# Kernel optimization log

Measured on AMD Instinct MI355X. Metric: run time of the kernel, lower is better.

## Reference

```python
import jax, jax.numpy as jnp
import numpy as np

B = 4096   # batch
C = 1024   # per-node channels


def setup_inputs() -> dict:
    key = jax.random.key(0)
    k0, k1, k2, k3, k4 = jax.random.split(key, 5)
    x0 = jax.random.normal(k0, (B, C), dtype=jnp.float32)
    x1 = jax.random.normal(k1, (B, C), dtype=jnp.float32)
    # per-edge DNet weights: edge_in=concat (2 heads -> 2C) -> matmul W -> edge_out=split (2 tails of C)
    scale = 0.02
    W0 = jax.random.normal(k2, (2 * C, 2 * C), dtype=jnp.float32) * scale
    W1 = jax.random.normal(k3, (2 * C, 2 * C), dtype=jnp.float32) * scale
    W2 = jax.random.normal(k4, (2 * C, 2 * C), dtype=jnp.float32) * scale
    return {"x0": x0, "x1": x1, "W0": W0, "W1": W1, "W2": W2}


def _edge(head_a, head_b, W):
    # MHD_concat over sorted head nodes (dim=1), DNet matmul, MHD_split into tail node channels
    z = jnp.concatenate([head_a, head_b], axis=1) @ W  # [B, 2C]
    return z[:, :C], z[:, C:]  # two tail tensors [B, C]


def reference(x0, x1, W0, W1, W2):
    # DAG routing in topological order (MHD_topological_sort of the role matrix):
    # edge0: heads (n0, n1) -> tails (n2, n3)
    # edge1: heads (n2, n3) -> tails (n4, n5)
    # edge2: heads (n4, n5) -> tails (n6, n7)
    # node_tail_func = 'sum' (single contribution per tail here)
    n2, n3 = _edge(x0, x1, W0)
    n4, n5 = _edge(n2, n3, W1)
    n6, n7 = _edge(n4, n5, W2)
    # output: concat of terminal nodes (sorted order)
    return jnp.concatenate([n6, n7], axis=1)  # [B, 2C]
```

## Files before the change

### kernel.cpp

```cpp
#include <hip/hip_runtime.h>
#include <hip/hip_bf16.h>
#include <stdint.h>

typedef __bf16 bf16;
typedef __bf16 bf16x8 __attribute__((ext_vector_type(8)));
typedef float f32x4 __attribute__((ext_vector_type(4)));

#define GAS __attribute__((address_space(1)))
#define LAS __attribute__((address_space(3)))

static constexpr int M = 4096;
static constexpr int N = 2048;
static constexpr int K = 2048;

static constexpr int BM = 128, BN = 256, BK = 64;
static constexpr int NT = K / BK;
static constexpr int A_ELE = BM * BK;
static constexpr int B_ELE = BN * BK;
static constexpr int BUF_ELE = A_ELE + B_ELE;

__device__ __forceinline__ void gload_lds16(const bf16* gsrc, bf16* ldst) {
    __builtin_amdgcn_global_load_lds((const GAS void*)gsrc, (LAS void*)ldst, 16, 0, 0);
}

__global__ __launch_bounds__(256) void prep_kernel(const float* __restrict__ x0,
                                                   const float* __restrict__ x1,
                                                   const float* __restrict__ W0,
                                                   const float* __restrict__ W1,
                                                   const float* __restrict__ W2,
                                                   bf16* __restrict__ A,
                                                   bf16* __restrict__ Wt0,
                                                   bf16* __restrict__ Wt1,
                                                   bf16* __restrict__ Wt2) {
    __shared__ bf16 tile[32][33];
    int bid = blockIdx.x;
    int tid = threadIdx.x;
    if (bid < 4096) {
        int idx = (bid * 256 + tid) * 8;
        int b = idx >> 11;
        int c = idx & 2047;
        const float* src = (c < 1024) ? (x0 + (size_t)b * 1024 + c)
                                      : (x1 + (size_t)b * 1024 + (c - 1024));
        float4 v0 = *reinterpret_cast<const float4*>(src);
        float4 v1 = *reinterpret_cast<const float4*>(src + 4);
        bf16x8 o;
        o[0] = (bf16)v0.x; o[1] = (bf16)v0.y; o[2] = (bf16)v0.z; o[3] = (bf16)v0.w;
        o[4] = (bf16)v1.x; o[5] = (bf16)v1.y; o[6] = (bf16)v1.z; o[7] = (bf16)v1.w;
        *reinterpret_cast<bf16x8*>(A + idx) = o;
    } else {
        int r = bid - 4096;
        int w = r >> 12;
        int t = r & 4095;
        const float* W  = (w == 0) ? W0  : (w == 1) ? W1  : W2;
        bf16*        Wt = (w == 0) ? Wt0 : (w == 1) ? Wt1 : Wt2;
        int n0 = (t & 63) * 32;
        int k0 = (t >> 6) * 32;
        int tx = tid & 31;
        int ty = tid >> 5;
        #pragma unroll
        for (int i = 0; i < 4; i++) {
            int k = ty + i * 8;
            tile[k][tx] = (bf16)W[(size_t)(k0 + k) * N + n0 + tx];
        }
        __syncthreads();
        #pragma unroll
        for (int i = 0; i < 4; i++) {
            int n = ty + i * 8;
            Wt[(size_t)(n0 + n) * K + k0 + tx] = tile[tx][n];
        }
    }
}

__device__ __forceinline__ void read_frags(const bf16* __restrict__ ba, const bf16* __restrict__ bb,
                                           int aoff, int boff, int slot,
                                           bf16x8 af[4], bf16x8 bv[4]) {
    #pragma unroll
    for (int mi = 0; mi < 4; mi++)
        af[mi] = *reinterpret_cast<const bf16x8*>(ba + aoff + mi * 1024 + slot);
    #pragma unroll
    for (int ni = 0; ni < 4; ni++)
        bv[ni] = *reinterpret_cast<const bf16x8*>(bb + boff + ni * 1024 + slot);
}

__device__ __forceinline__ void do_mfma16(const bf16x8 af[4], const bf16x8 bv[4], f32x4 acc[4][4]) {
    __builtin_amdgcn_s_setprio(1);
    #pragma unroll
    for (int mi = 0; mi < 4; mi++)
        #pragma unroll
        for (int ni = 0; ni < 4; ni++)
            acc[mi][ni] = __builtin_amdgcn_mfma_f32_16x16x32_bf16(af[mi], bv[ni], acc[mi][ni], 0, 0, 0);
    __builtin_amdgcn_s_setprio(0);
}

template <bool OUT_BF16>
__global__ __launch_bounds__(512, 2) void gemm1b_kernel(const bf16* __restrict__ A,
                                                        const bf16* __restrict__ Bt,
                                                        void* __restrict__ Cout) {
    __shared__ bf16 lds[3 * BUF_ELE];

    int bid = blockIdx.x;
    int cpx = gridDim.x >> 3;
    int swz = (bid & 7) * cpx + (bid >> 3);
    int tm = swz >> 3;
    int tn = swz & 7;

    int tid  = threadIdx.x;
    int wave = tid >> 6;
    int lane = tid & 63;
    int wr = wave >> 2;
    int wc = wave & 3;
    int fr = lane & 15;
    int fb = lane >> 4;

    int srow = wave * 8 + (lane >> 3);
    int scol = ((lane & 7) ^ (lane >> 3)) * 8;
    const bf16* aS = A  + (size_t)(tm * BM + srow) * K + scol;
    const bf16* bS = Bt + (size_t)(tn * BN + srow) * K + scol;
    int sdst = wave * 512;

    int aoff  = (wr * 64 + fr) * 64;
    int boff  = (wc * 64 + fr) * 64;
    int slot0 = ((fb) ^ (fr & 7)) * 8;
    int slot1 = ((4 | fb) ^ (fr & 7)) * 8;

    f32x4 acc[4][4] = {};

    auto STAGE = [&](int bi, int t) {
        bf16* ba = (bf16*)lds + bi * BUF_ELE;
        bf16* bb = ba + A_ELE;
        const bf16* a = aS + t * BK;
        const bf16* b = bS + t * BK;
        gload_lds16(a,           ba + sdst);
        gload_lds16(a + 64 * K,  ba + sdst + 4096);
        gload_lds16(b,           bb + sdst);
        gload_lds16(b + 64 * K,  bb + sdst + 4096);
        gload_lds16(b + 128 * K, bb + sdst + 8192);
        gload_lds16(b + 192 * K, bb + sdst + 12288);
    };

    STAGE(0, 0);
    STAGE(1, 1);
    asm volatile("s_waitcnt vmcnt(6)" ::: "memory");
    __builtin_amdgcn_s_barrier();

    bf16x8 af0[4], bv0[4], af1[4], bv1[4];
    int cur = 0;
    for (int t = 0; t < NT - 2; ++t) {
        const bf16* ba = (const bf16*)lds + cur * BUF_ELE;
        const bf16* bb = ba + A_ELE;
        int sb = cur + 2; if (sb >= 3) sb -= 3;

        read_frags(ba, bb, aoff, boff, slot0, af0, bv0);
        read_frags(ba, bb, aoff, boff, slot1, af1, bv1);
        STAGE(sb, t + 2);
        asm volatile("s_waitcnt lgkmcnt(8)" ::: "memory");
        do_mfma16(af0, bv0, acc);
        asm volatile("s_waitcnt lgkmcnt(0)" ::: "memory");
        do_mfma16(af1, bv1, acc);
        asm volatile("s_waitcnt vmcnt(6)" ::: "memory");
        __builtin_amdgcn_s_barrier();
        cur = cur + 1; if (cur >= 3) cur -= 3;
    }
    {
        const bf16* ba = (const bf16*)lds + cur * BUF_ELE;
        const bf16* bb = ba + A_ELE;
        read_frags(ba, bb, aoff, boff, slot0, af0, bv0);
        read_frags(ba, bb, aoff, boff, slot1, af1, bv1);
        asm volatile("s_waitcnt lgkmcnt(8)" ::: "memory");
        do_mfma16(af0, bv0, acc);
        asm volatile("s_waitcnt lgkmcnt(0)" ::: "memory");
        do_mfma16(af1, bv1, acc);
        asm volatile("s_waitcnt vmcnt(0)" ::: "memory");
        __builtin_amdgcn_s_barrier();
        cur = cur + 1; if (cur >= 3) cur -= 3;
    }
    {
        const bf16* ba = (const bf16*)lds + cur * BUF_ELE;
        const bf16* bb = ba + A_ELE;
        read_frags(ba, bb, aoff, boff, slot0, af0, bv0);
        read_frags(ba, bb, aoff, boff, slot1, af1, bv1);
        asm volatile("s_waitcnt lgkmcnt(8)" ::: "memory");
        do_mfma16(af0, bv0, acc);
        asm volatile("s_waitcnt lgkmcnt(0)" ::: "memory");
        do_mfma16(af1, bv1, acc);
    }

    int row0 = tm * BM + wr * 64 + (lane >> 4) * 4;
    int col0 = tn * BN + wc * 64 + (lane & 15);
    if constexpr (OUT_BF16) {
        bf16* C = (bf16*)Cout;
        #pragma unroll
        for (int mi = 0; mi < 4; mi++)
            #pragma unroll
            for (int r = 0; r < 4; r++) {
                size_t base = (size_t)(row0 + mi * 16 + r) * N + col0;
                #pragma unroll
                for (int ni = 0; ni < 4; ni++)
                    C[base + ni * 16] = (bf16)acc[mi][ni][r];
            }
    } else {
        float* C = (float*)Cout;
        #pragma unroll
        for (int mi = 0; mi < 4; mi++)
            #pragma unroll
            for (int r = 0; r < 4; r++) {
                size_t base = (size_t)(row0 + mi * 16 + r) * N + col0;
                #pragma unroll
                for (int ni = 0; ni < 4; ni++)
                    C[base + ni * 16] = acc[mi][ni][r];
            }
    }
}

extern "C" void kernel_launch(void* const* d_in, const int* in_sizes, int n_in,
                              void* d_out, int out_size, void* d_ws, size_t ws_size,
                              hipStream_t stream) {
    const float* x0 = (const float*)d_in[0];
    const float* x1 = (const float*)d_in[1];
    const float* W0 = (const float*)d_in[2];
    const float* W1 = (const float*)d_in[3];
    const float* W2 = (const float*)d_in[4];

    char* ws = (char*)d_ws;
    const size_t MB = 1024 * 1024;
    bf16* Wt0 = (bf16*)(ws + 0 * MB);
    bf16* Wt1 = (bf16*)(ws + 8 * MB);
    bf16* Wt2 = (bf16*)(ws + 16 * MB);

    bf16 *Apk, *z1, *z2;
    if (ws_size >= 56 * MB) {
        Apk = (bf16*)(ws + 24 * MB);
        z1  = (bf16*)(ws + 40 * MB);
        z2  = Apk;
    } else {
        Apk = (bf16*)d_out;
        z1  = (bf16*)d_out + (size_t)M * K;
        z2  = (bf16*)(ws + 24 * MB);
    }

    prep_kernel<<<4096 + 3 * 4096, 256, 0, stream>>>(x0, x1, W0, W1, W2, Apk, Wt0, Wt1, Wt2);

    constexpr int grid = (M / BM) * (N / BN);
    gemm1b_kernel<true ><<<grid, 512, 0, stream>>>(Apk, Wt0, z1);
    gemm1b_kernel<true ><<<grid, 512, 0, stream>>>(z1,  Wt1, z2);
    gemm1b_kernel<false><<<grid, 512, 0, stream>>>(z2,  Wt2, (float*)d_out);
}
```

Baseline: 123.5 us.

## Use 4-wave blocks with 64x128 per-wave tiles in chained GEMMs

The GEMM block shrinks from 8 waves to 4, and each wave now computes a 64x128 output sub-tile (4x8 MFMA accumulators) instead of 64x64. Global-to-LDS staging is reorganised so 256 threads issue 12 loads per stage, and sched_barriers pin the placement of the LDS fragment reads against the MFMA groups. The aim is more register-level reuse of A fragments and fewer LDS reads per MFMA. In exchange, accumulator register pressure doubles, launch bounds allow only one block per CU, and fewer waves are available to hide latency.

New measurement: 159.4 us. +29.1%, slower.

```diff
diff --git a/kernel.cpp b/kernel.cpp
--- a/kernel.cpp
+++ b/kernel.cpp
@@ -71,29 +71,29 @@
     }
 }
 
-__device__ __forceinline__ void read_frags(const bf16* __restrict__ ba, const bf16* __restrict__ bb,
-                                           int aoff, int boff, int slot,
-                                           bf16x8 af[4], bf16x8 bv[4]) {
+__device__ __forceinline__ void read_a(const bf16* __restrict__ ba, int aoff, int slot, bf16x8 af[4]) {
     #pragma unroll
     for (int mi = 0; mi < 4; mi++)
         af[mi] = *reinterpret_cast<const bf16x8*>(ba + aoff + mi * 1024 + slot);
+}
+__device__ __forceinline__ void read_b(const bf16* __restrict__ bb, int boff, int slot, bf16x8 bv[8]) {
     #pragma unroll
-    for (int ni = 0; ni < 4; ni++)
+    for (int ni = 0; ni < 8; ni++)
         bv[ni] = *reinterpret_cast<const bf16x8*>(bb + boff + ni * 1024 + slot);
 }
 
-__device__ __forceinline__ void do_mfma16(const bf16x8 af[4], const bf16x8 bv[4], f32x4 acc[4][4]) {
+__device__ __forceinline__ void do_mfma32(const bf16x8 af[4], const bf16x8 bv[8], f32x4 acc[4][8]) {
     __builtin_amdgcn_s_setprio(1);
     #pragma unroll
     for (int mi = 0; mi < 4; mi++)
         #pragma unroll
-        for (int ni = 0; ni < 4; ni++)
+        for (int ni = 0; ni < 8; ni++)
             acc[mi][ni] = __builtin_amdgcn_mfma_f32_16x16x32_bf16(af[mi], bv[ni], acc[mi][ni], 0, 0, 0);
     __builtin_amdgcn_s_setprio(0);
 }
 
 template <bool OUT_BF16>
-__global__ __launch_bounds__(512, 2) void gemm1b_kernel(const bf16* __restrict__ A,
+__global__ __launch_bounds__(256, 1) void gemm4w_kernel(const bf16* __restrict__ A,
                                                         const bf16* __restrict__ Bt,
                                                         void* __restrict__ Cout) {
     __shared__ bf16 lds[3 * BUF_ELE];
@@ -107,69 +107,77 @@
     int tid  = threadIdx.x;
     int wave = tid >> 6;
     int lane = tid & 63;
-    int wr = wave >> 2;
-    int wc = wave & 3;
+    int wr = wave >> 1;
+    int wc = wave & 1;
     int fr = lane & 15;
     int fb = lane >> 4;
 
-    int srow = wave * 8 + (lane >> 3);
-    int scol = ((lane & 7) ^ (lane >> 3)) * 8;
+    int srow = tid >> 3;
+    int scol = ((tid & 7) ^ (srow & 7)) * 8;
     const bf16* aS = A  + (size_t)(tm * BM + srow) * K + scol;
     const bf16* bS = Bt + (size_t)(tn * BN + srow) * K + scol;
     int sdst = wave * 512;
 
     int aoff  = (wr * 64 + fr) * 64;
-    int boff  = (wc * 64 + fr) * 64;
+    int boff  = (wc * 128 + fr) * 64;
     int slot0 = ((fb) ^ (fr & 7)) * 8;
     int slot1 = ((4 | fb) ^ (fr & 7)) * 8;
 
-    f32x4 acc[4][4] = {};
+    f32x4 acc[4][8] = {};
 
     auto STAGE = [&](int bi, int t) {
         bf16* ba = (bf16*)lds + bi * BUF_ELE;
         bf16* bb = ba + A_ELE;
         const bf16* a = aS + t * BK;
         const bf16* b = bS + t * BK;
-        gload_lds16(a,           ba + sdst);
-        gload_lds16(a + 64 * K,  ba + sdst + 4096);
-        gload_lds16(b,           bb + sdst);
-        gload_lds16(b + 64 * K,  bb + sdst + 4096);
-        gload_lds16(b + 128 * K, bb + sdst + 8192);
-        gload_lds16(b + 192 * K, bb + sdst + 12288);
+        #pragma unroll
+        for (int c = 0; c < 4; c++)
+            gload_lds16(a + (size_t)c * 32 * K, ba + sdst + c * 2048);
+        #pragma unroll
+        for (int c = 0; c < 8; c++)
+            gload_lds16(b + (size_t)c * 32 * K, bb + sdst + c * 2048);
     };
 
     STAGE(0, 0);
     STAGE(1, 1);
-    asm volatile("s_waitcnt vmcnt(6)" ::: "memory");
+    asm volatile("s_waitcnt vmcnt(12)" ::: "memory");
     __builtin_amdgcn_s_barrier();
 
-    bf16x8 af0[4], bv0[4], af1[4], bv1[4];
+    bf16x8 af0[4], bv0[8], af1[4], bv1[8];
     int cur = 0;
     for (int t = 0; t < NT - 2; ++t) {
         const bf16* ba = (const bf16*)lds + cur * BUF_ELE;
         const bf16* bb = ba + A_ELE;
         int sb = cur + 2; if (sb >= 3) sb -= 3;
 
-        read_frags(ba, bb, aoff, boff, slot0, af0, bv0);
-        read_frags(ba, bb, aoff, boff, slot1, af1, bv1);
+        read_a(ba, aoff, slot0, af0);
+        read_b(bb, boff, slot0, bv0);
         STAGE(sb, t + 2);
-        asm volatile("s_waitcnt lgkmcnt(8)" ::: "memory");
-        do_mfma16(af0, bv0, acc);
+        read_a(ba, aoff, slot1, af1);
+        read_b(bb, boff, slot1, bv1);
+        asm volatile("s_waitcnt lgkmcnt(12)" ::: "memory");
+        __builtin_amdgcn_sched_barrier(0);
+        do_mfma32(af0, bv0, acc);
         asm volatile("s_waitcnt lgkmcnt(0)" ::: "memory");
-        do_mfma16(af1, bv1, acc);
-        asm volatile("s_waitcnt vmcnt(6)" ::: "memory");
+        __builtin_amdgcn_sched_barrier(0);
+        do_mfma32(af1, bv1, acc);
+        asm volatile("s_waitcnt vmcnt(12)" ::: "memory");
         __builtin_amdgcn_s_barrier();
         cur = cur + 1; if (cur >= 3) cur -= 3;
     }
     {
         const bf16* ba = (const bf16*)lds + cur * BUF_ELE;
         const bf16* bb = ba + A_ELE;
-        read_frags(ba, bb, aoff, boff, slot0, af0, bv0);
-        read_frags(ba, bb, aoff, boff, slot1, af1, bv1);
-        asm volatile("s_waitcnt lgkmcnt(8)" ::: "memory");
-        do_mfma16(af0, bv0, acc);
+        read_a(ba, aoff, slot0, af0);
+        read_b(bb, boff, slot0, bv0);
+        read_a(ba, aoff, slot1, af1);
+        read_b(bb, boff, slot1, bv1);
+        asm volatile("s_waitcnt lgkmcnt(12)" ::: "memory");
+        __builtin_amdgcn_sched_barrier(0);
+        do_mfma32(af0, bv0, acc);
         asm volatile("s_waitcnt lgkmcnt(0)" ::: "memory");
-        do_mfma16(af1, bv1, acc);
+        __builtin_amdgcn_sched_barrier(0);
+        do_mfma32(af1, bv1, acc);
         asm volatile("s_waitcnt vmcnt(0)" ::: "memory");
         __builtin_amdgcn_s_barrier();
         cur = cur + 1; if (cur >= 3) cur -= 3;
@@ -177,16 +185,20 @@
     {
         const bf16* ba = (const bf16*)lds + cur * BUF_ELE;
         const bf16* bb = ba + A_ELE;
-        read_frags(ba, bb, aoff, boff, slot0, af0, bv0);
-        read_frags(ba, bb, aoff, boff, slot1, af1, bv1);
-        asm volatile("s_waitcnt lgkmcnt(8)" ::: "memory");
-        do_mfma16(af0, bv0, acc);
+        read_a(ba, aoff, slot0, af0);
+        read_b(bb, boff, slot0, bv0);
+        read_a(ba, aoff, slot1, af1);
+        read_b(bb, boff, slot1, bv1);
+        asm volatile("s_waitcnt lgkmcnt(12)" ::: "memory");
+        __builtin_amdgcn_sched_barrier(0);
+        do_mfma32(af0, bv0, acc);
         asm volatile("s_waitcnt lgkmcnt(0)" ::: "memory");
-        do_mfma16(af1, bv1, acc);
+        __builtin_amdgcn_sched_barrier(0);
+        do_mfma32(af1, bv1, acc);
     }
 
     int row0 = tm * BM + wr * 64 + (lane >> 4) * 4;
-    int col0 = tn * BN + wc * 64 + (lane & 15);
+    int col0 = tn * BN + wc * 128 + (lane & 15);
     if constexpr (OUT_BF16) {
         bf16* C = (bf16*)Cout;
         #pragma unroll
@@ -195,7 +207,7 @@
             for (int r = 0; r < 4; r++) {
                 size_t base = (size_t)(row0 + mi * 16 + r) * N + col0;
                 #pragma unroll
-                for (int ni = 0; ni < 4; ni++)
+                for (int ni = 0; ni < 8; ni++)
                     C[base + ni * 16] = (bf16)acc[mi][ni][r];
             }
     } else {
@@ -206,7 +218,7 @@
             for (int r = 0; r < 4; r++) {
                 size_t base = (size_t)(row0 + mi * 16 + r) * N + col0;
                 #pragma unroll
-                for (int ni = 0; ni < 4; ni++)
+                for (int ni = 0; ni < 8; ni++)
                     C[base + ni * 16] = acc[mi][ni][r];
             }
     }
@@ -241,7 +253,7 @@
     prep_kernel<<<4096 + 3 * 4096, 256, 0, stream>>>(x0, x1, W0, W1, W2, Apk, Wt0, Wt1, Wt2);
 
     constexpr int grid = (M / BM) * (N / BN);
-    gemm1b_kernel<true ><<<grid, 512, 0, stream>>>(Apk, Wt0, z1);
-    gemm1b_kernel<true ><<<grid, 512, 0, stream>>>(z1,  Wt1, z2);
-    gemm1b_kernel<false><<<grid, 512, 0, stream>>>(z2,  Wt2, (float*)d_out);
-}
+    gemm4w_kernel<true ><<<grid, 256, 0, stream>>>(Apk, Wt0, z1);
+    gemm4w_kernel<true ><<<grid, 256, 0, stream>>>(z1,  Wt1, z2);
+    gemm4w_kernel<false><<<grid, 256, 0, stream>>>(z2,  Wt2, (float*)d_out);
+}
```

## Reassociate chained matmuls to precompute combined weight W0·W1·W2

Applied to the files above, without the earlier changes.

Instead of pushing the 4096-row activation through three sequential 2048x2048 GEMMs, the launcher first multiplies the weights together. Two smaller weight-by-weight GEMMs produce the transposed product W0·W1·W2, then one activation GEMM applies it. A new 64x128-tile gemmw kernel handles the 2048x2048 products, and the prep kernel now packs W0 without transposing it. This cuts total FLOPs by roughly a third. The trade-off is an extra bf16 rounding of the combined weight, which changes the numerical error profile. Scheduling barriers are also added between the MFMA groups.

New measurement: 101.1 us. -18.1%, faster.

```diff
diff --git a/kernel.cpp b/kernel.cpp
--- a/kernel.cpp
+++ b/kernel.cpp
@@ -19,6 +19,10 @@
 static constexpr int B_ELE = BN * BK;
 static constexpr int BUF_ELE = A_ELE + B_ELE;
 
+static constexpr int WA_ELE = 64 * BK;
+static constexpr int WB_ELE = 128 * BK;
+static constexpr int WBUF_ELE = WA_ELE + WB_ELE;
+
 __device__ __forceinline__ void gload_lds16(const bf16* gsrc, bf16* ldst) {
     __builtin_amdgcn_global_load_lds((const GAS void*)gsrc, (LAS void*)ldst, 16, 0, 0);
 }
@@ -28,10 +32,10 @@
                                                    const float* __restrict__ W0,
                                                    const float* __restrict__ W1,
                                                    const float* __restrict__ W2,
-                                                   bf16* __restrict__ A,
-                                                   bf16* __restrict__ Wt0,
-                                                   bf16* __restrict__ Wt1,
-                                                   bf16* __restrict__ Wt2) {
+                                                   bf16* __restrict__ Xpk,
+                                                   bf16* __restrict__ W0pk,
+                                                   bf16* __restrict__ W1t,
+                                                   bf16* __restrict__ W2t) {
     __shared__ bf16 tile[32][33];
     int bid = blockIdx.x;
     int tid = threadIdx.x;
@@ -46,13 +50,21 @@
         bf16x8 o;
         o[0] = (bf16)v0.x; o[1] = (bf16)v0.y; o[2] = (bf16)v0.z; o[3] = (bf16)v0.w;
         o[4] = (bf16)v1.x; o[5] = (bf16)v1.y; o[6] = (bf16)v1.z; o[7] = (bf16)v1.w;
-        *reinterpret_cast<bf16x8*>(A + idx) = o;
+        *reinterpret_cast<bf16x8*>(Xpk + idx) = o;
+    } else if (bid < 6144) {
+        int idx = ((bid - 4096) * 256 + tid) * 8;
+        float4 v0 = *reinterpret_cast<const float4*>(W0 + idx);
+        float4 v1 = *reinterpret_cast<const float4*>(W0 + idx + 4);
+        bf16x8 o;
+        o[0] = (bf16)v0.x; o[1] = (bf16)v0.y; o[2] = (bf16)v0.z; o[3] = (bf16)v0.w;
+        o[4] = (bf16)v1.x; o[5] = (bf16)v1.y; o[6] = (bf16)v1.z; o[7] = (bf16)v1.w;
+        *reinterpret_cast<bf16x8*>(W0pk + idx) = o;
     } else {
-        int r = bid - 4096;
+        int r = bid - 6144;
         int w = r >> 12;
         int t = r & 4095;
-        const float* W  = (w == 0) ? W0  : (w == 1) ? W1  : W2;
-        bf16*        Wt = (w == 0) ? Wt0 : (w == 1) ? Wt1 : Wt2;
+        const float* W  = (w == 0) ? W1  : W2;
+        bf16*        Wt = (w == 0) ? W1t : W2t;
         int n0 = (t & 63) * 32;
         int k0 = (t >> 6) * 32;
         int tx = tid & 31;
@@ -92,10 +104,9 @@
     __builtin_amdgcn_s_setprio(0);
 }
 
-template <bool OUT_BF16>
-__global__ __launch_bounds__(512, 2) void gemm1b_kernel(const bf16* __restrict__ A,
-                                                        const bf16* __restrict__ Bt,
-                                                        void* __restrict__ Cout) {
+__global__ __launch_bounds__(512, 2) void gemmx_kernel(const bf16* __restrict__ A,
+                                                       const bf16* __restrict__ Bt,
+                                                       float* __restrict__ Cout) {
     __shared__ bf16 lds[3 * BUF_ELE];
 
     int bid = blockIdx.x;
@@ -154,8 +165,10 @@
         read_frags(ba, bb, aoff, boff, slot1, af1, bv1);
         STAGE(sb, t + 2);
         asm volatile("s_waitcnt lgkmcnt(8)" ::: "memory");
+        __builtin_amdgcn_sched_barrier(0);
         do_mfma16(af0, bv0, acc);
         asm volatile("s_waitcnt lgkmcnt(0)" ::: "memory");
+        __builtin_amdgcn_sched_barrier(0);
         do_mfma16(af1, bv1, acc);
         asm volatile("s_waitcnt vmcnt(6)" ::: "memory");
         __builtin_amdgcn_s_barrier();
@@ -167,8 +180,10 @@
         read_frags(ba, bb, aoff, boff, slot0, af0, bv0);
         read_frags(ba, bb, aoff, boff, slot1, af1, bv1);
         asm volatile("s_waitcnt lgkmcnt(8)" ::: "memory");
+        __builtin_amdgcn_sched_barrier(0);
         do_mfma16(af0, bv0, acc);
         asm volatile("s_waitcnt lgkmcnt(0)" ::: "memory");
+        __builtin_amdgcn_sched_barrier(0);
         do_mfma16(af1, bv1, acc);
         asm volatile("s_waitcnt vmcnt(0)" ::: "memory");
         __builtin_amdgcn_s_barrier();
@@ -180,36 +195,152 @@
         read_frags(ba, bb, aoff, boff, slot0, af0, bv0);
         read_frags(ba, bb, aoff, boff, slot1, af1, bv1);
         asm volatile("s_waitcnt lgkmcnt(8)" ::: "memory");
+        __builtin_amdgcn_sched_barrier(0);
         do_mfma16(af0, bv0, acc);
         asm volatile("s_waitcnt lgkmcnt(0)" ::: "memory");
+        __builtin_amdgcn_sched_barrier(0);
         do_mfma16(af1, bv1, acc);
     }
 
     int row0 = tm * BM + wr * 64 + (lane >> 4) * 4;
     int col0 = tn * BN + wc * 64 + (lane & 15);
-    if constexpr (OUT_BF16) {
-        bf16* C = (bf16*)Cout;
-        #pragma unroll
-        for (int mi = 0; mi < 4; mi++)
+    #pragma unroll
+    for (int mi = 0; mi < 4; mi++)
+        #pragma unroll
+        for (int r = 0; r < 4; r++) {
+            size_t base = (size_t)(row0 + mi * 16 + r) * N + col0;
             #pragma unroll
-            for (int r = 0; r < 4; r++) {
-                size_t base = (size_t)(row0 + mi * 16 + r) * N + col0;
-                #pragma unroll
-                for (int ni = 0; ni < 4; ni++)
-                    C[base + ni * 16] = (bf16)acc[mi][ni][r];
-            }
-    } else {
-        float* C = (float*)Cout;
-        #pragma unroll
-        for (int mi = 0; mi < 4; mi++)
+            for (int ni = 0; ni < 4; ni++)
+                Cout[base + ni * 16] = acc[mi][ni][r];
+        }
+}
+
+__global__ __launch_bounds__(256, 2) void gemmw_kernel(const bf16* __restrict__ A,
+                                                       const bf16* __restrict__ Bt,
+                                                       bf16* __restrict__ C) {
+    __shared__ bf16 lds[3 * WBUF_ELE];
+
+    int bid = blockIdx.x;
+    int cpx = gridDim.x >> 3;
+    int swz = (bid & 7) * cpx + (bid >> 3);
+    int tm = swz >> 4;
+    int tn = swz & 15;
+
+    int tid  = threadIdx.x;
+    int wave = tid >> 6;
+    int lane = tid & 63;
+    int wr = wave >> 1;
+    int wc = wave & 1;
+    int fr = lane & 15;
+    int fb = lane >> 4;
+
+    int srow = tid >> 3;
+    int scol = ((tid & 7) ^ (srow & 7)) * 8;
+    const bf16* aS = A  + (size_t)(tm * 64  + srow) * K + scol;
+    const bf16* bS = Bt + (size_t)(tn * 128 + srow) * K + scol;
+    int sdst = wave * 512;
+
+    int aoff  = (wr * 32 + fr) * 64;
+    int boff  = (wc * 64 + fr) * 64;
+    int slot0 = ((fb) ^ (fr & 7)) * 8;
+    int slot1 = ((4 | fb) ^ (fr & 7)) * 8;
+
+    f32x4 acc[2][4] = {};
+
+    auto STAGE = [&](int bi, int t) {
+        bf16* ba = (bf16*)lds + bi * WBUF_ELE;
+        bf16* bb = ba + WA_ELE;
+        const bf16* a = aS + t * BK;
+        const bf16* b = bS + t * BK;
+        gload_lds16(a,          ba + sdst);
+        gload_lds16(a + 32 * K, ba + sdst + 2048);
+        #pragma unroll
+        for (int c = 0; c < 4; c++)
+            gload_lds16(b + (size_t)c * 32 * K, bb + sdst + c * 2048);
+    };
+
+    auto READ = [&](const bf16* ba, const bf16* bb, int slot, bf16x8 af[2], bf16x8 bv[4]) {
+        af[0] = *reinterpret_cast<const bf16x8*>(ba + aoff + slot);
+        af[1] = *reinterpret_cast<const bf16x8*>(ba + aoff + 1024 + slot);
+        #pragma unroll
+        for (int ni = 0; ni < 4; ni++)
+            bv[ni] = *reinterpret_cast<const bf16x8*>(bb + boff + ni * 1024 + slot);
+    };
+
+    auto MFMA8 = [&](const bf16x8 af[2], const bf16x8 bv[4]) {
+        __builtin_amdgcn_s_setprio(1);
+        #pragma unroll
+        for (int mi = 0; mi < 2; mi++)
             #pragma unroll
-            for (int r = 0; r < 4; r++) {
-                size_t base = (size_t)(row0 + mi * 16 + r) * N + col0;
-                #pragma unroll
-                for (int ni = 0; ni < 4; ni++)
-                    C[base + ni * 16] = acc[mi][ni][r];
-            }
-    }
+            for (int ni = 0; ni < 4; ni++)
+                acc[mi][ni] = __builtin_amdgcn_mfma_f32_16x16x32_bf16(af[mi], bv[ni], acc[mi][ni], 0, 0, 0);
+        __builtin_amdgcn_s_setprio(0);
+    };
+
+    STAGE(0, 0);
+    STAGE(1, 1);
+    asm volatile("s_waitcnt vmcnt(6)" ::: "memory");
+    __builtin_amdgcn_s_barrier();
+
+    bf16x8 af0[2], bv0[4], af1[2], bv1[4];
+    int cur = 0;
+    for (int t = 0; t < NT - 2; ++t) {
+        const bf16* ba = (const bf16*)lds + cur * WBUF_ELE;
+        const bf16* bb = ba + WA_ELE;
+        int sb = cur + 2; if (sb >= 3) sb -= 3;
+
+        READ(ba, bb, slot0, af0, bv0);
+        READ(ba, bb, slot1, af1, bv1);
+        STAGE(sb, t + 2);
+        asm volatile("s_waitcnt lgkmcnt(6)" ::: "memory");
+        __builtin_amdgcn_sched_barrier(0);
+        MFMA8(af0, bv0);
+        asm volatile("s_waitcnt lgkmcnt(0)" ::: "memory");
+        __builtin_amdgcn_sched_barrier(0);
+        MFMA8(af1, bv1);
+        asm volatile("s_waitcnt vmcnt(6)" ::: "memory");
+        __builtin_amdgcn_s_barrier();
+        cur = cur + 1; if (cur >= 3) cur -= 3;
+    }
+    {
+        const bf16* ba = (const bf16*)lds + cur * WBUF_ELE;
+        const bf16* bb = ba + WA_ELE;
+        READ(ba, bb, slot0, af0, bv0);
+        READ(ba, bb, slot1, af1, bv1);
+        asm volatile("s_waitcnt lgkmcnt(6)" ::: "memory");
+        __builtin_amdgcn_sched_barrier(0);
+        MFMA8(af0, bv0);
+        asm volatile("s_waitcnt lgkmcnt(0)" ::: "memory");
+        __builtin_amdgcn_sched_barrier(0);
+        MFMA8(af1, bv1);
+        asm volatile("s_waitcnt vmcnt(0)" ::: "memory");
+        __builtin_amdgcn_s_barrier();
+        cur = cur + 1; if (cur >= 3) cur -= 3;
+    }
+    {
+        const bf16* ba = (const bf16*)lds + cur * WBUF_ELE;
+        const bf16* bb = ba + WA_ELE;
+        READ(ba, bb, slot0, af0, bv0);
+        READ(ba, bb, slot1, af1, bv1);
+        asm volatile("s_waitcnt lgkmcnt(6)" ::: "memory");
+        __builtin_amdgcn_sched_barrier(0);
+        MFMA8(af0, bv0);
+        asm volatile("s_waitcnt lgkmcnt(0)" ::: "memory");
+        __builtin_amdgcn_sched_barrier(0);
+        MFMA8(af1, bv1);
+    }
+
+    int row0 = tm * 64 + wr * 32 + (lane >> 4) * 4;
+    int col0 = tn * 128 + wc * 64 + fr;
+    #pragma unroll
+    for (int mi = 0; mi < 2; mi++)
+        #pragma unroll
+        for (int r = 0; r < 4; r++) {
+            size_t base = (size_t)(row0 + mi * 16 + r) * 2048 + col0;
+            #pragma unroll
+            for (int ni = 0; ni < 4; ni++)
+                C[base + ni * 16] = (bf16)acc[mi][ni][r];
+        }
 }
 
 extern "C" void kernel_launch(void* const* d_in, const int* in_sizes, int n_in,
@@ -223,25 +354,17 @@
 
     char* ws = (char*)d_ws;
     const size_t MB = 1024 * 1024;
-    bf16* Wt0 = (bf16*)(ws + 0 * MB);
-    bf16* Wt1 = (bf16*)(ws + 8 * MB);
-    bf16* Wt2 = (bf16*)(ws + 16 * MB);
-
-    bf16 *Apk, *z1, *z2;
-    if (ws_size >= 56 * MB) {
-        Apk = (bf16*)(ws + 24 * MB);
-        z1  = (bf16*)(ws + 40 * MB);
-        z2  = Apk;
-    } else {
-        Apk = (bf16*)d_out;
-        z1  = (bf16*)d_out + (size_t)M * K;
-        z2  = (bf16*)(ws + 24 * MB);
-    }
-
-    prep_kernel<<<4096 + 3 * 4096, 256, 0, stream>>>(x0, x1, W0, W1, W2, Apk, Wt0, Wt1, Wt2);
-
-    constexpr int grid = (M / BM) * (N / BN);
-    gemm1b_kernel<true ><<<grid, 512, 0, stream>>>(Apk, Wt0, z1);
-    gemm1b_kernel<true ><<<grid, 512, 0, stream>>>(z1,  Wt1, z2);
-    gemm1b_kernel<false><<<grid, 512, 0, stream>>>(z2,  Wt2, (float*)d_out);
-}
+    bf16* Xpk    = (bf16*)(ws + 0 * MB);
+    bf16* W1t    = (bf16*)(ws + 16 * MB);
+    bf16* W012t  = (bf16*)(ws + 16 * MB);
+    bf16* W2t    = (bf16*)(ws + 24 * MB);
+    bf16* W01    = (bf16*)(ws + 32 * MB);
+    bf16* W0pk   = (bf16*)d_out;
+
+    prep_kernel<<<4096 + 2048 + 2 * 4096, 256, 0, stream>>>(x0, x1, W0, W1, W2,
+                                                            Xpk, W0pk, W1t, W2t);
+
+    gemmw_kernel<<<(2048 / 64) * (2048 / 128), 256, 0, stream>>>(W0pk, W1t, W01);
+    gemmw_kernel<<<(2048 / 64) * (2048 / 128), 256, 0, stream>>>(W2t, W01, W012t);
+    gemmx_kernel<<<(M / BM) * (N / BN), 512, 0, stream>>>(Xpk, W012t, (float*)d_out);
+}
```
